# Performance work log

Measured on AMD Instinct MI355X. Metric: run time of the kernel, lower is better.

## Reference

```python
import jax, jax.numpy as jnp
import numpy as np

R = 40            # guided-filter radius (81x81 window)
EPS = 1e-3
BETA = 2.996 / 300.0  # visibility_m = 300.0


def _box_sum(x, r=R):
    """Zero-padded sliding-window sum over an (B,C,H,W) tensor.
    Matches F.avg_pool2d(x, 2r+1, stride=1, padding=r) * (2r+1)^2
    (count_include_pad=True), computed in O(HW) via prefix sums."""
    B, C, H, W = x.shape

    def _along(y, axis, L):
        cs = jnp.cumsum(y, axis=axis)
        pad = [(0, 0)] * 4
        pad[axis] = (1, 0)
        cs = jnp.pad(cs, pad)  # cs[i] = sum of first i elements
        hi = jnp.clip(jnp.arange(L) + r + 1, 0, L)
        lo = jnp.clip(jnp.arange(L) - r, 0, L)
        return jnp.take(cs, hi, axis=axis) - jnp.take(cs, lo, axis=axis)

    x = _along(x, 2, H)
    x = _along(x, 3, W)
    return x


def _guided_filter(I, p, r=R, eps=EPS):
    N = (2 * r + 1) ** 2
    mean_I = _box_sum(I, r) / N
    mean_p = _box_sum(p, r) / N
    mean_Ip = _box_sum(I * p, r) / N
    cov_Ip = mean_Ip - mean_I * mean_p
    mean_II = _box_sum(I * I, r) / N
    var_I = mean_II - mean_I * mean_I
    a = cov_Ip / (var_I + eps)
    b = mean_p - a * mean_I
    mean_a = _box_sum(a, r) / N
    mean_b = _box_sum(b, r) / N
    return mean_a * I + mean_b


def setup_inputs() -> dict:
    key = jax.random.key(0)
    k1, k2 = jax.random.split(key)
    B, H, W = 8, 768, 1280
    img = jax.random.uniform(k1, (B, 3, H, W), dtype=jnp.float32)
    depth = jax.random.uniform(k2, (B, 1, H, W), dtype=jnp.float32) * 500.0
    return {"img": img, "depth": depth}


def reference(img, depth):
    B, _, H, W = img.shape
    t_raw = jnp.clip(jnp.exp(-BETA * depth), 0.0, 1.0)          # (B,1,H,W)
    gray = (0.299 * img[:, 0:1] + 0.587 * img[:, 1:2]
            + 0.114 * img[:, 2:3])                               # (B,1,H,W)
    t = _guided_filter(gray, t_raw)                               # (B,1,H,W)

    # atmospheric light A: mean color over the k farthest pixels, per image
    k = max(10, int(0.001 * H * W))
    k = min(k, H * W)
    depth_flat = depth.reshape(B, -1)                             # (B,HW)
    img_flat = img.reshape(B, 3, -1)                              # (B,3,HW)
    _, idx = jax.lax.top_k(depth_flat, k)                         # (B,k)
    A = jnp.take_along_axis(img_flat, idx[:, None, :], axis=2).mean(axis=2)
    A = A.reshape(B, 3, 1, 1)

    return img * t + A * (1.0 - t)
```

## Files before the change

### kernel.cpp

```cpp
#include <hip/hip_runtime.h>
#include <hip/hip_fp16.h>
#include <stdint.h>

typedef unsigned int u32;

#define Bn 8
#define Hn 768
#define Wn 1280
#define HWs (Hn*Wn)
#define Rr 40
#define NNinv (1.0f/6561.0f)
#define KTOP 983
#define BETA_C (2.996f/300.0f)
#define EQCAP 4096
#define TK_BPI 480
#define NCH 96
#define SEGV 16
#define NSEGV 48
#define HIMG 4
#define TK1_WAVES 16
#define TW 640
#define CW 680

#define OFF_F     0
#define OFF_AB1   (16*HWs)
#define OFF_AB2   (24*HWs)
#define OFF_CS4f  (32*HWs)
#define OFF_CS2f  (36*HWs)
#define OFF_TAILf (38*HWs)

#define OFFH_FOVF 0
#define OFFH_AB   (4*HWs)
#define CS_N      (HIMG*NCH*Wn)
#define OFFH_CS4  (12*HWs)
#define OFFH_CS2  (OFFH_CS4 + 4*CS_N)
#define OFFH_TAIL (OFFH_CS2 + 2*CS_N)

#define ZERO_U32  (Bn*4096 + Bn*65536 + Bn)
#define ZERO_U4   (ZERO_U32/4)

__device__ __forceinline__ float4 f4add(float4 a, float4 b){ return make_float4(a.x+b.x,a.y+b.y,a.z+b.z,a.w+b.w); }
__device__ __forceinline__ float4 f4sub(float4 a, float4 b){ return make_float4(a.x-b.x,a.y-b.y,a.z-b.z,a.w-b.w); }

__device__ __forceinline__ u32 h2_to_u32(__half2 h){ union { __half2 h; u32 u; } c; c.h = h; return c.u; }
__device__ __forceinline__ __half2 u32_to_h2(u32 u){ union { u32 u; __half2 h; } c; c.u = u; return c.h; }

__global__ __launch_bounds__(256) void fill0_kernel(uint4* __restrict__ p){
  int i = blockIdx.x*256 + threadIdx.x;
  if (i < ZERO_U4) p[i] = make_uint4(0,0,0,0);
}


__global__ __launch_bounds__(256) void gA_kernel(const float* __restrict__ img, const float* __restrict__ depth,
    uint2* __restrict__ F, float4* __restrict__ CS4){
  __shared__ float4 lds[769];
  __shared__ float4 wtot[4];
  int blk = blockIdx.x;
  int xt = blk & 1;
  int t2 = blk >> 1;
  int b = t2 / NCH, ch = t2 % NCH;
  int x0 = xt*TW;
  int cstart = xt ? (TW - Rr) : 0;
  int tid = threadIdx.x;
  int lane = tid & 63, wv = tid >> 6;
  float4 acc[3];
  #pragma unroll
  for (int j = 0; j < 3; ++j) acc[j] = make_float4(0,0,0,0);
  for (int r = 0; r < 8; ++r){
    int y = ch*8 + r;
    const float* ir = img + ((size_t)(b*3+0)*Hn + y)*Wn + cstart;
    const float* ig = img + ((size_t)(b*3+1)*Hn + y)*Wn + cstart;
    const float* ib = img + ((size_t)(b*3+2)*Hn + y)*Wn + cstart;
    const float* dp = depth + ((size_t)b*Hn + y)*Wn + cstart;
    __syncthreads();
    for (int i = tid; i < 768; i += 256){
      if (i < CW){
        float rr = ir[i], g = ig[i], bb = ib[i];
        float I = 0.299f*rr + 0.587f*g + 0.114f*bb;
        float p = expf(-BETA_C*dp[i]);
        p = fminf(fmaxf(p, 0.0f), 1.0f);
        lds[i] = make_float4(I, p, I*p, I*I);
      } else {
        lds[i] = make_float4(0,0,0,0);
      }
    }
    __syncthreads();
    int base = tid*3;
    float4 loc[3]; float4 tsum = make_float4(0,0,0,0);
    #pragma unroll
    for (int j = 0; j < 3; ++j){ loc[j] = lds[base+j]; tsum = f4add(tsum, loc[j]); }
    float4 v = tsum;
    for (int d = 1; d < 64; d <<= 1){
      float4 o; o.x = __shfl_up(v.x, d); o.y = __shfl_up(v.y, d); o.z = __shfl_up(v.z, d); o.w = __shfl_up(v.w, d);
      if (lane >= d) v = f4add(v, o);
    }
    if (lane == 63) wtot[wv] = v;
    __syncthreads();
    float4 ex = f4sub(v, tsum);
    for (int w = 0; w < wv; ++w) ex = f4add(ex, wtot[w]);
    float4 run = ex;
    #pragma unroll
    for (int j = 0; j < 3; ++j){ lds[base+j] = run; run = f4add(run, loc[j]); }
    __syncthreads();
    #pragma unroll
    for (int j = 0; j < 3; ++j){
      int lx = tid + j*256;
      if (lx < TW){
        int gx = x0 + lx;
        int hi = gx + Rr + 1; if (hi > Wn) hi = Wn;
        int lo = gx - Rr;     if (lo < 0)  lo = 0;
        float4 s = f4sub(lds[hi - cstart], lds[lo - cstart]);
        __half2 h01 = __float22half2_rn(make_float2(s.x, s.y));
        __half2 h23 = __float22half2_rn(make_float2(s.z, s.w));
        F[(size_t)b*HWs + (size_t)y*Wn + gx] = make_uint2(h2_to_u32(h01), h2_to_u32(h23));
        float2 f0 = __half22float2(h01), f1 = __half22float2(h23);
        acc[j] = f4add(acc[j], make_float4(f0.x, f0.y, f1.x, f1.y));
      }
    }
  }
  #pragma unroll
  for (int j = 0; j < 3; ++j){
    int lx = tid + j*256;
    if (lx < TW) CS4[((size_t)b*NCH + ch)*Wn + x0 + lx] = acc[j];
  }
}

__global__ __launch_bounds__(256) void vAf_kernel(const uint2* __restrict__ F, const float4* __restrict__ CS,
    u32* __restrict__ AB){
  int gt = blockIdx.x*256 + threadIdx.x;
  int x  = gt % Wn;
  int t2 = gt / Wn;
  int b = t2 % Bn, s = t2 / Bn;
  const uint2* Fb   = F + (size_t)b*HWs;
  const float4* CSb = CS + (size_t)b*NCH*Wn;
  int y0 = s*SEGV;
  int c0 = 2*s - 5; if (c0 < 0) c0 = 0;
  int c1 = 2*s + 5; if (c1 > NCH) c1 = NCH;
  float4 S = make_float4(0,0,0,0);
  for (int c = c0; c < c1; ++c) S = f4add(S, CSb[(size_t)c*Wn + x]);
  u32* ABb = AB + (size_t)b*HWs;
  #pragma unroll 2
  for (int y = y0; y < y0 + SEGV; ++y){
    int ya = y + Rr;
    if (ya < Hn){
      uint2 u = Fb[(size_t)ya*Wn + x];
      float2 f0 = __half22float2(u32_to_h2(u.x)), f1 = __half22float2(u32_to_h2(u.y));
      S.x += f0.x; S.y += f0.y; S.z += f1.x; S.w += f1.y;
    }
    float mI = S.x*NNinv, mp = S.y*NNinv, mIp = S.z*NNinv, mII = S.w*NNinv;
    float var = mII - mI*mI;
    float a  = (mIp - mI*mp) / (var + 1e-3f);
    float bb = mp - a*mI;
    ABb[(size_t)y*Wn + x] = h2_to_u32(__float22half2_rn(make_float2(a, bb)));
    int yb = y - Rr;
    if (yb >= 0){
      uint2 u = Fb[(size_t)yb*Wn + x];
      float2 f0 = __half22float2(u32_to_h2(u.x)), f1 = __half22float2(u32_to_h2(u.y));
      S.x -= f0.x; S.y -= f0.y; S.z -= f1.x; S.w -= f1.y;
    }
  }
}

__global__ __launch_bounds__(256) void gB_kernel(const u32* __restrict__ AB1, u32* __restrict__ AB2,
    float2* __restrict__ CS2){
  __shared__ float2 lds[769];
  __shared__ float2 wtot[4];
  int blk = blockIdx.x;
  int xt = blk & 1;
  int t2 = blk >> 1;
  int b = t2 / NCH, ch = t2 % NCH;
  int x0 = xt*TW;
  int cstart = xt ? (TW - Rr) : 0;
  int tid = threadIdx.x;
  int lane = tid & 63, wv = tid >> 6;
  float2 acc[3];
  #pragma unroll
  for (int j = 0; j < 3; ++j) acc[j] = make_float2(0,0);
  for (int r = 0; r < 8; ++r){
    int y = ch*8 + r;
    const u32* row = AB1 + (size_t)b*HWs + (size_t)y*Wn + cstart;
    __syncthreads();
    for (int i = tid; i < 768; i += 256){
      if (i < CW) lds[i] = __half22float2(u32_to_h2(row[i]));
      else        lds[i] = make_float2(0,0);
    }
    __syncthreads();
    int base = tid*3;
    float2 loc[3]; float2 tsum = make_float2(0,0);
    #pragma unroll
    for (int j = 0; j < 3; ++j){ loc[j] = lds[base+j]; tsum.x += loc[j].x; tsum.y += loc[j].y; }
    float2 v = tsum;
    for (int d = 1; d < 64; d <<= 1){
      float2 o; o.x = __shfl_up(v.x, d); o.y = __shfl_up(v.y, d);
      if (lane >= d){ v.x += o.x; v.y += o.y; }
    }
    if (lane == 63) wtot[wv] = v;
    __syncthreads();
    float2 ex = make_float2(v.x - tsum.x, v.y - tsum.y);
    for (int w = 0; w < wv; ++w){ ex.x += wtot[w].x; ex.y += wtot[w].y; }
    float2 run = ex;
    #pragma unroll
    for (int j = 0; j < 3; ++j){ lds[base+j] = run; run.x += loc[j].x; run.y += loc[j].y; }
    __syncthreads();
    #pragma unroll
    for (int j = 0; j < 3; ++j){
      int lx = tid + j*256;
      if (lx < TW){
        int gx = x0 + lx;
        int hi = gx + Rr + 1; if (hi > Wn) hi = Wn;
        int lo = gx - Rr;     if (lo < 0)  lo = 0;
        float2 s = make_float2(lds[hi - cstart].x - lds[lo - cstart].x,
                               lds[hi - cstart].y - lds[lo - cstart].y);
        __half2 h = __float22half2_rn(s);
        AB2[(size_t)b*HWs + (size_t)y*Wn + gx] = h2_to_u32(h);
        float2 fr = __half22float2(h);
        acc[j].x += fr.x; acc[j].y += fr.y;
      }
    }
  }
  #pragma unroll
  for (int j = 0; j < 3; ++j){
    int lx = tid + j*256;
    if (lx < TW) CS2[((size_t)b*NCH + ch)*Wn + x0 + lx] = acc[j];
  }
}

__global__ __launch_bounds__(256) void vBf_kernel(const u32* __restrict__ AB2, const float2* __restrict__ CS,
    const float* __restrict__ img, const float* __restrict__ Avec, float* __restrict__ out){
  int gt = blockIdx.x*256 + threadIdx.x;
  int x  = gt % Wn;
  int t2 = gt / Wn;
  int b = t2 % Bn, s = t2 / Bn;
  const u32* ABb = AB2 + (size_t)b*HWs;
  const float2* CSb = CS + (size_t)b*NCH*Wn;
  int y0 = s*SEGV;
  int c0 = 2*s - 5; if (c0 < 0) c0 = 0;
  int c1 = 2*s + 5; if (c1 > NCH) c1 = NCH;
  float2 S = make_float2(0,0);
  for (int c = c0; c < c1; ++c){ float2 t = CSb[(size_t)c*Wn + x]; S.x += t.x; S.y += t.y; }
  float A0 = Avec[b*3+0], A1 = Avec[b*3+1], A2 = Avec[b*3+2];
  const float* ir = img + (size_t)(b*3+0)*HWs;
  const float* ig = img + (size_t)(b*3+1)*HWs;
  const float* ib = img + (size_t)(b*3+2)*HWs;
  float* o0 = out + (size_t)(b*3+0)*HWs;
  float* o1 = out + (size_t)(b*3+1)*HWs;
  float* o2 = out + (size_t)(b*3+2)*HWs;
  #pragma unroll 2
  for (int y = y0; y < y0 + SEGV; ++y){
    int ya = y + Rr;
    if (ya < Hn){ float2 t = __half22float2(u32_to_h2(ABb[(size_t)ya*Wn + x])); S.x += t.x; S.y += t.y; }
    float ma = S.x*NNinv, mb = S.y*NNinv;
    size_t idx = (size_t)y*Wn + x;
    float r = ir[idx], g = ig[idx], bb = ib[idx];
    float gray = 0.299f*r + 0.587f*g + 0.114f*bb;
    float t = ma*gray + mb;
    o0[idx] = r *t + A0*(1.0f - t);
    o1[idx] = g *t + A1*(1.0f - t);
    o2[idx] = bb*t + A2*(1.0f - t);
    int yb = y - Rr;
    if (yb >= 0){ float2 t2v = __half22float2(u32_to_h2(ABb[(size_t)yb*Wn + x])); S.x -= t2v.x; S.y -= t2v.y; }
  }
}


__global__ __launch_bounds__(256) void hA_kernel(const float* __restrict__ img, const float* __restrict__ depth,
    float4* __restrict__ Fd, float4* __restrict__ Fw, int half){
  __shared__ float4 lds[Wn+1];
  __shared__ float4 wtot[4];
  int blk = blockIdx.x;
  int bl = blk / Hn, y = blk % Hn;
  int b = half*HIMG + bl;
  const float* ir = img + ((size_t)(b*3+0)*Hn + y)*Wn;
  const float* ig = img + ((size_t)(b*3+1)*Hn + y)*Wn;
  const float* ib = img + ((size_t)(b*3+2)*Hn + y)*Wn;
  const float* dp = depth + ((size_t)b*Hn + y)*Wn;
  int tid = threadIdx.x;
  for (int i = tid; i < Wn; i += 256){
    float r = ir[i], g = ig[i], bb = ib[i];
    float I = 0.299f*r + 0.587f*g + 0.114f*bb;
    float p = expf(-BETA_C*dp[i]);
    p = fminf(fmaxf(p, 0.0f), 1.0f);
    lds[i] = make_float4(I, p, I*p, I*I);
  }
  __syncthreads();
  float4 loc[5]; float4 tsum = make_float4(0,0,0,0);
  for (int j = 0; j < 5; ++j){ loc[j] = lds[tid*5+j]; tsum = f4add(tsum, loc[j]); }
  int lane = tid & 63, wv = tid >> 6;
  float4 v = tsum;
  for (int d = 1; d < 64; d <<= 1){
    float4 o; o.x = __shfl_up(v.x, d); o.y = __shfl_up(v.y, d); o.z = __shfl_up(v.z, d); o.w = __shfl_up(v.w, d);
    if (lane >= d) v = f4add(v, o);
  }
  if (lane == 63) wtot[wv] = v;
  __syncthreads();
  float4 ex = f4sub(v, tsum);
  for (int w = 0; w < wv; ++w) ex = f4add(ex, wtot[w]);
  float4 run = ex;
  for (int j = 0; j < 5; ++j){ lds[tid*5+j] = run; run = f4add(run, loc[j]); }
  if (tid == 255) lds[Wn] = run;
  __syncthreads();
  float4* F = (bl < 3) ? (Fd + (size_t)bl*HWs) : Fw;
  for (int j = 0; j < 5; ++j){
    int xx = tid + j*256;
    int hi = xx + Rr + 1; if (hi > Wn) hi = Wn;
    int lo = xx - Rr;     if (lo < 0)  lo = 0;
    F[(size_t)y*Wn + xx] = f4sub(lds[hi], lds[lo]);
  }
}

__global__ __launch_bounds__(256) void cs4_kernel(const float4* __restrict__ Fd, const float4* __restrict__ Fw,
    float4* __restrict__ CS){
  int gt = blockIdx.x*256 + threadIdx.x;
  int x  = gt % Wn;
  int t2 = gt / Wn;
  int bl = t2 % HIMG, ch = t2 / HIMG;
  const float4* F = (bl < 3) ? (Fd + (size_t)bl*HWs) : Fw;
  const float4* p = F + (size_t)ch*8*Wn + x;
  float4 s = make_float4(0,0,0,0);
  #pragma unroll
  for (int i = 0; i < 8; ++i) s = f4add(s, p[(size_t)i*Wn]);
  CS[((size_t)bl*NCH + ch)*Wn + x] = s;
}

__global__ __launch_bounds__(256) void vA_kernel(const float4* __restrict__ Fd, const float4* __restrict__ Fw,
    const float4* __restrict__ CS, float2* __restrict__ AB){
  int gt = blockIdx.x*256 + threadIdx.x;
  int x  = gt % Wn;
  int t2 = gt / Wn;
  int bl = t2 % HIMG, s = t2 / HIMG;
  const float4* F   = (bl < 3) ? (Fd + (size_t)bl*HWs) : Fw;
  const float4* CSb = CS + (size_t)bl*NCH*Wn;
  int y0 = s*SEGV;
  int c0 = 2*s - 5; if (c0 < 0) c0 = 0;
  int c1 = 2*s + 5; if (c1 > NCH) c1 = NCH;
  float4 S = make_float4(0,0,0,0);
  for (int c = c0; c < c1; ++c) S = f4add(S, CSb[(size_t)c*Wn + x]);
  float2* ABb = AB + (size_t)bl*HWs;
  #pragma unroll 2
  for (int y = y0; y < y0 + SEGV; ++y){
    int ya = y + Rr;
    if (ya < Hn) S = f4add(S, F[(size_t)ya*Wn + x]);
    float mI = S.x*NNinv, mp = S.y*NNinv, mIp = S.z*NNinv, mII = S.w*NNinv;
    float var = mII - mI*mI;
    float a  = (mIp - mI*mp) / (var + 1e-3f);
    float bb = mp - a*mI;
    ABb[(size_t)y*Wn + x] = make_float2(a, bb);
    int yb = y - Rr;
    if (yb >= 0) S = f4sub(S, F[(size_t)yb*Wn + x]);
  }
}

__global__ __launch_bounds__(256) void hB_kernel(float2* __restrict__ AB){
  __shared__ float2 lds[Wn+1];
  __shared__ float2 wtot[4];
  int blk = blockIdx.x;
  int bl = blk / Hn, y = blk % Hn;
  float2* row = AB + ((size_t)bl*Hn + y)*Wn;
  int tid = threadIdx.x;
  for (int i = tid; i < Wn; i += 256) lds[i] = row[i];
  __syncthreads();
  float2 loc[5]; float2 tsum = make_float2(0,0);
  for (int j = 0; j < 5; ++j){ loc[j] = lds[tid*5+j]; tsum.x += loc[j].x; tsum.y += loc[j].y; }
  int lane = tid & 63, wv = tid >> 6;
  float2 v = tsum;
  for (int d = 1; d < 64; d <<= 1){
    float2 o; o.x = __shfl_up(v.x, d); o.y = __shfl_up(v.y, d);
    if (lane >= d){ v.x += o.x; v.y += o.y; }
  }
  if (lane == 63) wtot[wv] = v;
  __syncthreads();
  float2 ex = make_float2(v.x - tsum.x, v.y - tsum.y);
  for (int w = 0; w < wv; ++w){ ex.x += wtot[w].x; ex.y += wtot[w].y; }
  float2 run = ex;
  for (int j = 0; j < 5; ++j){ lds[tid*5+j] = run; run.x += loc[j].x; run.y += loc[j].y; }
  if (tid == 255) lds[Wn] = run;
  __syncthreads();
  for (int j = 0; j < 5; ++j){
    int xx = tid + j*256;
    int hi = xx + Rr + 1; if (hi > Wn) hi = Wn;
    int lo = xx - Rr;     if (lo < 0)  lo = 0;
    row[xx] = make_float2(lds[hi].x - lds[lo].x, lds[hi].y - lds[lo].y);
  }
}

__global__ __launch_bounds__(256) void cs2_kernel(const float2* __restrict__ AB, float2* __restrict__ CS){
  int gt = blockIdx.x*256 + threadIdx.x;
  int x  = gt % Wn;
  int t2 = gt / Wn;
  int bl = t2 % HIMG, ch = t2 / HIMG;
  const float2* p = AB + (size_t)bl*HWs + (size_t)ch*8*Wn + x;
  float2 s = make_float2(0,0);
  #pragma unroll
  for (int i = 0; i < 8; ++i){ s.x += p[(size_t)i*Wn].x; s.y += p[(size_t)i*Wn].y; }
  CS[((size_t)bl*NCH + ch)*Wn + x] = s;
}

__global__ __launch_bounds__(256) void vB_kernel(const float2* __restrict__ AB, const float2* __restrict__ CS,
    const float* __restrict__ img, const float* __restrict__ Avec, float* __restrict__ out, int half){
  int gt = blockIdx.x*256 + threadIdx.x;
  int x  = gt % Wn;
  int t2 = gt / Wn;
  int bl = t2 % HIMG, s = t2 / HIMG;
  int b = half*HIMG + bl;
  const float2* ABb = AB + (size_t)bl*HWs;
  const float2* CSb = CS + (size_t)bl*NCH*Wn;
  int y0 = s*SEGV;
  int c0 = 2*s - 5; if (c0 < 0) c0 = 0;
  int c1 = 2*s + 5; if (c1 > NCH) c1 = NCH;
  float2 S = make_float2(0,0);
  for (int c = c0; c < c1; ++c){ float2 t = CSb[(size_t)c*Wn + x]; S.x += t.x; S.y += t.y; }
  float A0 = Avec[b*3+0], A1 = Avec[b*3+1], A2 = Avec[b*3+2];
  const float* ir = img + (size_t)(b*3+0)*HWs;
  const float* ig = img + (size_t)(b*3+1)*HWs;
  const float* ib = img + (size_t)(b*3+2)*HWs;
  float* o0 = out + (size_t)(b*3+0)*HWs;
  float* o1 = out + (size_t)(b*3+1)*HWs;
  float* o2 = out + (size_t)(b*3+2)*HWs;
  #pragma unroll 2
  for (int y = y0; y < y0 + SEGV; ++y){
    int ya = y + Rr;
    if (ya < Hn){ float2 t = ABb[(size_t)ya*Wn + x]; S.x += t.x; S.y += t.y; }
    float ma = S.x*NNinv, mb = S.y*NNinv;
    size_t idx = (size_t)y*Wn + x;
    float r = ir[idx], g = ig[idx], bb = ib[idx];
    float gray = 0.299f*r + 0.587f*g + 0.114f*bb;
    float t = ma*gray + mb;
    o0[idx] = r *t + A0*(1.0f - t);
    o1[idx] = g *t + A1*(1.0f - t);
    o2[idx] = bb*t + A2*(1.0f - t);
    int yb = y - Rr;
    if (yb >= 0){ float2 t2v = ABb[(size_t)yb*Wn + x]; S.x -= t2v.x; S.y -= t2v.y; }
  }
}


__global__ __launch_bounds__(1024) void tk1_kernel(const float* __restrict__ depth, u32* __restrict__ hist1){
  __shared__ u32 lh[TK1_WAVES*2048];
  int tid = threadIdx.x;
  for (int i = tid; i < TK1_WAVES*2048; i += 1024) lh[i] = 0;
  __syncthreads();
  int b = blockIdx.x >> 5;
  int slice = blockIdx.x & 31;
  const int per = HWs/32;
  int start = b*HWs + slice*per;
  u32* h = &lh[(tid >> 6) * 2048];
  const float2* dp = (const float2*)(depth + start);
  for (int i = tid; i < per/2; i += 1024){
    float2 v = dp[i];
    u32 u0 = __float_as_uint(v.x), u1 = __float_as_uint(v.y);
    u32 b0 = u0 >> 20, b1 = u1 >> 20;
    atomicAdd(&h[b0 >> 1], (b0 & 1u) ? 65536u : 1u);
    atomicAdd(&h[b1 >> 1], (b1 & 1u) ? 65536u : 1u);
  }
  __syncthreads();
  for (int i = tid; i < 4096; i += 1024){
    u32 s = 0;
    for (int w = 0; w < TK1_WAVES; ++w) s += (lh[w*2048 + (i>>1)] >> ((i&1)*16)) & 0xFFFFu;
    if (s) atomicAdd(&hist1[b*4096+i], s);
  }
}

__global__ __launch_bounds__(256) void tk2_kernel(const u32* __restrict__ hist1,
    u32* __restrict__ selP1, u32* __restrict__ selK1){
  int b = blockIdx.x, tid = threadIdx.x;
  const u32* h = hist1 + b*4096;
  u32 cs = 0; int bb = tid*16;
  for (int i = 0; i < 16; ++i) cs += h[bb+i];
  __shared__ u32 sums[256];
  sums[tid] = cs; __syncthreads();
  u32 above = 0;
  for (int t = tid+1; t < 256; ++t) above += sums[t];
  if (above < KTOP && above + cs >= KTOP){
    u32 acc = above;
    for (int i = 15; i >= 0; --i){
      u32 c = h[bb+i]; acc += c;
      if (acc >= KTOP){ selP1[b] = (u32)(bb+i); selK1[b] = KTOP - (acc - c); break; }
    }
  }
}

__global__ __launch_bounds__(256) void tk3_kernel(const float* __restrict__ depth,
    const u32* __restrict__ selP1, u32* __restrict__ hist2){
  int idx = blockIdx.x*2048 + threadIdx.x;
  int b = blockIdx.x / TK_BPI;
  u32 p1 = selP1[b];
  for (int it = 0; it < 8; ++it, idx += 256){
    u32 u = __float_as_uint(depth[idx]);
    if ((u>>20) == p1) atomicAdd(&hist2[b*65536 + ((u>>4)&0xFFFFu)], 1u);
  }
}

__global__ __launch_bounds__(256) void tk4_kernel(const u32* __restrict__ hist2, const u32* __restrict__ selP1,
    const u32* __restrict__ selK1, u32* __restrict__ selTau, u32* __restrict__ selK2){
  int b = blockIdx.x, tid = threadIdx.x;
  const u32* h = hist2 + b*65536;
  u32 kk = selK1[b];
  u32 cs = 0; int bb = tid*256;
  for (int i = 0; i < 256; ++i) cs += h[bb+i];
  __shared__ u32 sums[256];
  sums[tid] = cs; __syncthreads();
  u32 above = 0;
  for (int t = tid+1; t < 256; ++t) above += sums[t];
  if (above < kk && above + cs >= kk){
    u32 acc = above;
    for (int i = 255; i >= 0; --i){
      u32 c = h[bb+i]; acc += c;
      if (acc >= kk){ selTau[b] = (selP1[b]<<16) | (u32)(bb+i); selK2[b] = kk - (acc - c); break; }
    }
  }
}

__global__ __launch_bounds__(256) void tk5_kernel(const float* __restrict__ depth, const float* __restrict__ img,
    const u32* __restrict__ selTau, u32* __restrict__ eqCount, u32* __restrict__ eqVal, u32* __restrict__ eqIdx,
    float* __restrict__ partial){
  int blk = blockIdx.x;
  int b = blk / TK_BPI;
  u32 tau = selTau[b];
  int idx = blk*2048 + threadIdx.x;
  float cr = 0.f, cg = 0.f, cb = 0.f;
  for (int it = 0; it < 8; ++it, idx += 256){
    int pix = idx - b*HWs;
    u32 u = __float_as_uint(depth[idx]);
    u32 u28 = u >> 4;
    if (u28 > tau){
      cr += img[(size_t)(b*3+0)*HWs + pix];
      cg += img[(size_t)(b*3+1)*HWs + pix];
      cb += img[(size_t)(b*3+2)*HWs + pix];
    } else if (u28 == tau){
      u32 p = atomicAdd(&eqCount[b], 1u);
      if (p < EQCAP){ eqVal[b*EQCAP+p] = u; eqIdx[b*EQCAP+p] = (u32)pix; }
    }
  }
  for (int d = 32; d; d >>= 1){
    cr += __shfl_down(cr, d); cg += __shfl_down(cg, d); cb += __shfl_down(cb, d);
  }
  __shared__ float wsum[4][3];
  int lane = threadIdx.x & 63, wv = threadIdx.x >> 6;
  if (lane == 0){ wsum[wv][0] = cr; wsum[wv][1] = cg; wsum[wv][2] = cb; }
  __syncthreads();
  if (threadIdx.x == 0){
    float r = 0.f, g = 0.f, bl = 0.f;
    for (int w = 0; w < 4; ++w){ r += wsum[w][0]; g += wsum[w][1]; bl += wsum[w][2]; }
    partial[blk*3+0] = r; partial[blk*3+1] = g; partial[blk*3+2] = bl;
  }
}

__global__ void tk6_kernel(const float* __restrict__ img, const u32* __restrict__ eqCount,
    u32* __restrict__ eqVal, const u32* __restrict__ eqIdx, const u32* __restrict__ selK2,
    const float* __restrict__ partial, float* __restrict__ Avec){
  int b = blockIdx.x;
  int tid = threadIdx.x;
  float r = 0.f, g = 0.f, bl = 0.f;
  for (int i = tid; i < TK_BPI; i += 64){
    r  += partial[(b*TK_BPI+i)*3+0];
    g  += partial[(b*TK_BPI+i)*3+1];
    bl += partial[(b*TK_BPI+i)*3+2];
  }
  for (int d = 32; d; d >>= 1){
    r += __shfl_down(r, d); g += __shfl_down(g, d); bl += __shfl_down(bl, d);
  }
  if (tid != 0) return;
  u32 m = eqCount[b]; if (m > EQCAP) m = EQCAP;
  u32 need = selK2[b]; if (need > m) need = m;
  float cr = r, cg = g, cb = bl;
  for (u32 it = 0; it < need; ++it){
    int best = -1; u32 bv = 0, bi = 0;
    for (u32 j = 0; j < m; ++j){
      u32 vv = eqVal[b*EQCAP+j];
      if (vv == 0xFFFFFFFFu) continue;
      u32 ix = eqIdx[b*EQCAP+j];
      if (best < 0 || vv > bv || (vv == bv && ix < bi)){ best = (int)j; bv = vv; bi = ix; }
    }
    eqVal[b*EQCAP+best] = 0xFFFFFFFFu;
    cr += img[(size_t)(b*3+0)*HWs + bi];
    cg += img[(size_t)(b*3+1)*HWs + bi];
    cb += img[(size_t)(b*3+2)*HWs + bi];
  }
  float inv = 1.0f/(float)KTOP;
  Avec[b*3+0] = cr*inv; Avec[b*3+1] = cg*inv; Avec[b*3+2] = cb*inv;
}


extern "C" void kernel_launch(void* const* d_in, const int* in_sizes, int n_in,
                              void* d_out, int out_size, void* d_ws, size_t ws_size,
                              hipStream_t stream){
  const float* img   = (const float*)d_in[0];
  const float* depth = (const float*)d_in[1];
  float* out = (float*)d_out;
  float* ws  = (float*)d_ws;

  const size_t tailFloats = (size_t)ZERO_U32 + 4*Bn + 2*(size_t)Bn*EQCAP
                          + (size_t)Bn*TK_BPI*3 + Bn*3 + 16;
  const size_t needFull = ((size_t)38*HWs + tailFloats) * sizeof(float);
  bool full = (ws_size >= needFull);

  size_t offTail = full ? (size_t)OFF_TAILf : (size_t)OFFH_TAIL;
  u32* tail    = (u32*)(ws + offTail);
  u32* hist1   = tail;
  u32* hist2   = hist1 + Bn*4096;
  u32* eqCount = hist2 + (size_t)Bn*65536;
  u32* selP1   = eqCount + Bn;
  u32* selK1   = selP1 + Bn;
  u32* selTau  = selK1 + Bn;
  u32* selK2   = selTau + Bn;
  u32* eqVal   = selK2 + Bn;
  u32* eqIdx   = eqVal + (size_t)Bn*EQCAP;
  float* partial = (float*)(eqIdx + (size_t)Bn*EQCAP);
  float* Avec    = partial + (size_t)Bn*TK_BPI*3;

  fill0_kernel<<<dim3((ZERO_U4 + 255)/256), dim3(256), 0, stream>>>((uint4*)tail);

  tk1_kernel<<<dim3(Bn*32), dim3(1024), 0, stream>>>(depth, hist1);
  tk2_kernel<<<dim3(Bn),    dim3(256), 0, stream>>>(hist1, selP1, selK1);
  tk3_kernel<<<dim3(Bn*TK_BPI), dim3(256), 0, stream>>>(depth, selP1, hist2);
  tk4_kernel<<<dim3(Bn),    dim3(256), 0, stream>>>(hist2, selP1, selK1, selTau, selK2);
  tk5_kernel<<<dim3(Bn*TK_BPI), dim3(256), 0, stream>>>(depth, img, selTau, eqCount, eqVal, eqIdx, partial);
  tk6_kernel<<<dim3(Bn),    dim3(64),  0, stream>>>(img, eqCount, eqVal, eqIdx, selK2, partial, Avec);

  if (full){
    uint2*  F   = (uint2*)(ws + OFF_F);
    u32*    AB1 = (u32*)(ws + OFF_AB1);
    u32*    AB2 = (u32*)(ws + OFF_AB2);
    float4* CS4 = (float4*)(ws + OFF_CS4f);
    float2* CS2 = (float2*)(ws + OFF_CS2f);
    gA_kernel <<<dim3(Bn*NCH*2),            dim3(256), 0, stream>>>(img, depth, F, CS4);
    vAf_kernel<<<dim3((Bn*Wn*NSEGV)/256),   dim3(256), 0, stream>>>(F, CS4, AB1);
    gB_kernel <<<dim3(Bn*NCH*2),            dim3(256), 0, stream>>>(AB1, AB2, CS2);
    vBf_kernel<<<dim3((Bn*Wn*NSEGV)/256),   dim3(256), 0, stream>>>(AB2, CS2, img, Avec, out);
  } else {
    float4* Fw  = (float4*)(ws + OFFH_FOVF);
    float2* AB  = (float2*)(ws + OFFH_AB);
    float4* CS4 = (float4*)(ws + OFFH_CS4);
    float2* CS2 = (float2*)(ws + OFFH_CS2);
    for (int half = 0; half < 2; ++half){
      float4* Fd = (float4*)out + (size_t)half*3*HWs;
      hA_kernel <<<dim3(HIMG*Hn),            dim3(256), 0, stream>>>(img, depth, Fd, Fw, half);
      cs4_kernel<<<dim3((HIMG*NCH*Wn)/256),  dim3(256), 0, stream>>>(Fd, Fw, CS4);
      vA_kernel <<<dim3((HIMG*Wn*NSEGV)/256),dim3(256), 0, stream>>>(Fd, Fw, CS4, AB);
      hB_kernel <<<dim3(HIMG*Hn),            dim3(256), 0, stream>>>(AB);
      cs2_kernel<<<dim3((HIMG*NCH*Wn)/256),  dim3(256), 0, stream>>>(AB, CS2);
      vB_kernel <<<dim3((HIMG*Wn*NSEGV)/256),dim3(256), 0, stream>>>(AB, CS2, img, Avec, out, half);
    }
  }
}
```

Measured before the change: 234.9 us.

## Compact top-k candidates in pass 3 and vectorize guided-filter input loads

The third top-k pass now also accumulates colour sums for pixels whose coarse bin is above the threshold. It compacts the pixels that fall in the threshold bin into a per-image candidate list through an LDS stage and one global atomic per block. The fifth pass then scans only that short candidate list with far fewer blocks, instead of re-reading the whole depth map. This removes a full depth pass and most of the image gathers, at the cost of more workspace for candidate buffers and extra atomics in tk3. Separately, gA loads image and depth as float2, with two pixels per thread, and zeroes the LDS tail in one step.

Result: slower. 250.0 us (+6.4%).

```diff
diff --git a/kernel.cpp b/kernel.cpp
--- a/kernel.cpp
+++ b/kernel.cpp
@@ -14,6 +14,9 @@
 #define BETA_C (2.996f/300.0f)
 #define EQCAP 4096
 #define TK_BPI 480
+#define TK5_BPI 64
+#define TK_PART (TK_BPI + TK5_BPI)
+#define CAND_CAP HWs
 #define NCH 96
 #define SEGV 16
 #define NSEGV 48
@@ -36,7 +39,7 @@
 #define OFFH_CS2  (OFFH_CS4 + 4*CS_N)
 #define OFFH_TAIL (OFFH_CS2 + 2*CS_N)
 
-#define ZERO_U32  (Bn*4096 + Bn*65536 + Bn)
+#define ZERO_U32  (Bn*4096 + Bn*65536 + Bn + Bn*32)
 #define ZERO_U4   (ZERO_U32/4)
 
 __device__ __forceinline__ float4 f4add(float4 a, float4 b){ return make_float4(a.x+b.x,a.y+b.y,a.z+b.z,a.w+b.w); }
@@ -68,22 +71,21 @@
   for (int j = 0; j < 3; ++j) acc[j] = make_float4(0,0,0,0);
   for (int r = 0; r < 8; ++r){
     int y = ch*8 + r;
-    const float* ir = img + ((size_t)(b*3+0)*Hn + y)*Wn + cstart;
-    const float* ig = img + ((size_t)(b*3+1)*Hn + y)*Wn + cstart;
-    const float* ib = img + ((size_t)(b*3+2)*Hn + y)*Wn + cstart;
-    const float* dp = depth + ((size_t)b*Hn + y)*Wn + cstart;
-    __syncthreads();
-    for (int i = tid; i < 768; i += 256){
-      if (i < CW){
-        float rr = ir[i], g = ig[i], bb = ib[i];
-        float I = 0.299f*rr + 0.587f*g + 0.114f*bb;
-        float p = expf(-BETA_C*dp[i]);
-        p = fminf(fmaxf(p, 0.0f), 1.0f);
-        lds[i] = make_float4(I, p, I*p, I*I);
-      } else {
-        lds[i] = make_float4(0,0,0,0);
-      }
-    }
+    const float2* ir2 = (const float2*)(img + ((size_t)(b*3+0)*Hn + y)*Wn + cstart);
+    const float2* ig2 = (const float2*)(img + ((size_t)(b*3+1)*Hn + y)*Wn + cstart);
+    const float2* ib2 = (const float2*)(img + ((size_t)(b*3+2)*Hn + y)*Wn + cstart);
+    const float2* dp2 = (const float2*)(depth + ((size_t)b*Hn + y)*Wn + cstart);
+    __syncthreads();
+    for (int i = tid; i < 340; i += 256){
+      float2 r2 = ir2[i], g2 = ig2[i], b2 = ib2[i], d2 = dp2[i];
+      float I0 = 0.299f*r2.x + 0.587f*g2.x + 0.114f*b2.x;
+      float I1 = 0.299f*r2.y + 0.587f*g2.y + 0.114f*b2.y;
+      float e0 = fminf(fmaxf(expf(-BETA_C*d2.x), 0.0f), 1.0f);
+      float e1 = fminf(fmaxf(expf(-BETA_C*d2.y), 0.0f), 1.0f);
+      lds[2*i]   = make_float4(I0, e0, I0*e0, I0*I0);
+      lds[2*i+1] = make_float4(I1, e1, I1*e1, I1*I1);
+    }
+    if (tid < 88) lds[680+tid] = make_float4(0,0,0,0);
     __syncthreads();
     int base = tid*3;
     float4 loc[3]; float4 tsum = make_float4(0,0,0,0);
@@ -479,14 +481,54 @@
   }
 }
 
-__global__ __launch_bounds__(256) void tk3_kernel(const float* __restrict__ depth,
-    const u32* __restrict__ selP1, u32* __restrict__ hist2){
-  int idx = blockIdx.x*2048 + threadIdx.x;
-  int b = blockIdx.x / TK_BPI;
+__global__ __launch_bounds__(256) void tk3_kernel(const float* __restrict__ depth, const float* __restrict__ img,
+    const u32* __restrict__ selP1, u32* __restrict__ hist2,
+    u32* __restrict__ candU, u32* __restrict__ candP, u32* __restrict__ candCnt,
+    float* __restrict__ partial){
+  __shared__ u32 lu[2048], lp[2048];
+  __shared__ u32 lcnt, gbase;
+  int blk = blockIdx.x;
+  int b = blk / TK_BPI;
+  int tid = threadIdx.x;
+  if (tid == 0) lcnt = 0;
+  __syncthreads();
   u32 p1 = selP1[b];
+  int idx = blk*2048 + tid;
+  float cr = 0.f, cg = 0.f, cb = 0.f;
   for (int it = 0; it < 8; ++it, idx += 256){
+    int pix = idx - b*HWs;
     u32 u = __float_as_uint(depth[idx]);
-    if ((u>>20) == p1) atomicAdd(&hist2[b*65536 + ((u>>4)&0xFFFFu)], 1u);
+    u32 bin = u >> 20;
+    if (bin > p1){
+      cr += img[(size_t)(b*3+0)*HWs + pix];
+      cg += img[(size_t)(b*3+1)*HWs + pix];
+      cb += img[(size_t)(b*3+2)*HWs + pix];
+    } else if (bin == p1){
+      atomicAdd(&hist2[b*65536 + ((u>>4)&0xFFFFu)], 1u);
+      u32 pos = atomicAdd(&lcnt, 1u);
+      lu[pos] = u; lp[pos] = (u32)pix;
+    }
+  }
+  __syncthreads();
+  if (tid == 0) gbase = atomicAdd(&candCnt[b*32], lcnt);
+  __syncthreads();
+  u32 n = lcnt, base = gbase;
+  for (u32 i = tid; i < n; i += 256){
+    candU[(size_t)b*CAND_CAP + base + i] = lu[i];
+    candP[(size_t)b*CAND_CAP + base + i] = lp[i];
+  }
+  for (int d = 32; d; d >>= 1){
+    cr += __shfl_down(cr, d); cg += __shfl_down(cg, d); cb += __shfl_down(cb, d);
+  }
+  __shared__ float wsum[4][3];
+  int lane = tid & 63, wv = tid >> 6;
+  if (lane == 0){ wsum[wv][0] = cr; wsum[wv][1] = cg; wsum[wv][2] = cb; }
+  __syncthreads();
+  if (tid == 0){
+    float r = 0.f, g = 0.f, bl = 0.f;
+    for (int w = 0; w < 4; ++w){ r += wsum[w][0]; g += wsum[w][1]; bl += wsum[w][2]; }
+    int slot = b*TK_PART + (blk - b*TK_BPI);
+    partial[slot*3+0] = r; partial[slot*3+1] = g; partial[slot*3+2] = bl;
   }
 }
 
@@ -510,17 +552,18 @@
   }
 }
 
-__global__ __launch_bounds__(256) void tk5_kernel(const float* __restrict__ depth, const float* __restrict__ img,
+__global__ __launch_bounds__(256) void tk5_kernel(const float* __restrict__ img,
+    const u32* __restrict__ candU, const u32* __restrict__ candP, const u32* __restrict__ candCnt,
     const u32* __restrict__ selTau, u32* __restrict__ eqCount, u32* __restrict__ eqVal, u32* __restrict__ eqIdx,
     float* __restrict__ partial){
-  int blk = blockIdx.x;
-  int b = blk / TK_BPI;
+  int b = blockIdx.x / TK5_BPI;
+  int lb = blockIdx.x % TK5_BPI;
   u32 tau = selTau[b];
-  int idx = blk*2048 + threadIdx.x;
+  u32 cnt = candCnt[b*32]; if (cnt > CAND_CAP) cnt = CAND_CAP;
   float cr = 0.f, cg = 0.f, cb = 0.f;
-  for (int it = 0; it < 8; ++it, idx += 256){
-    int pix = idx - b*HWs;
-    u32 u = __float_as_uint(depth[idx]);
+  for (u32 i = lb*256 + threadIdx.x; i < cnt; i += TK5_BPI*256){
+    u32 u = candU[(size_t)b*CAND_CAP + i];
+    u32 pix = candP[(size_t)b*CAND_CAP + i];
     u32 u28 = u >> 4;
     if (u28 > tau){
       cr += img[(size_t)(b*3+0)*HWs + pix];
@@ -528,7 +571,7 @@
       cb += img[(size_t)(b*3+2)*HWs + pix];
     } else if (u28 == tau){
       u32 p = atomicAdd(&eqCount[b], 1u);
-      if (p < EQCAP){ eqVal[b*EQCAP+p] = u; eqIdx[b*EQCAP+p] = (u32)pix; }
+      if (p < EQCAP){ eqVal[b*EQCAP+p] = u; eqIdx[b*EQCAP+p] = pix; }
     }
   }
   for (int d = 32; d; d >>= 1){
@@ -541,7 +584,8 @@
   if (threadIdx.x == 0){
     float r = 0.f, g = 0.f, bl = 0.f;
     for (int w = 0; w < 4; ++w){ r += wsum[w][0]; g += wsum[w][1]; bl += wsum[w][2]; }
-    partial[blk*3+0] = r; partial[blk*3+1] = g; partial[blk*3+2] = bl;
+    int slot = b*TK_PART + TK_BPI + lb;
+    partial[slot*3+0] = r; partial[slot*3+1] = g; partial[slot*3+2] = bl;
   }
 }
 
@@ -551,10 +595,10 @@
   int b = blockIdx.x;
   int tid = threadIdx.x;
   float r = 0.f, g = 0.f, bl = 0.f;
-  for (int i = tid; i < TK_BPI; i += 64){
-    r  += partial[(b*TK_BPI+i)*3+0];
-    g  += partial[(b*TK_BPI+i)*3+1];
-    bl += partial[(b*TK_BPI+i)*3+2];
+  for (int i = tid; i < TK_PART; i += 64){
+    r  += partial[(b*TK_PART+i)*3+0];
+    g  += partial[(b*TK_PART+i)*3+1];
+    bl += partial[(b*TK_PART+i)*3+2];
   }
   for (int d = 32; d; d >>= 1){
     r += __shfl_down(r, d); g += __shfl_down(g, d); bl += __shfl_down(bl, d);
@@ -590,7 +634,8 @@
   float* ws  = (float*)d_ws;
 
   const size_t tailFloats = (size_t)ZERO_U32 + 4*Bn + 2*(size_t)Bn*EQCAP
-                          + (size_t)Bn*TK_BPI*3 + Bn*3 + 16;
+                          + (size_t)Bn*TK_PART*3 + Bn*3
+                          + 2*(size_t)Bn*CAND_CAP + 16;
   const size_t needFull = ((size_t)38*HWs + tailFloats) * sizeof(float);
   bool full = (ws_size >= needFull);
 
@@ -599,22 +644,25 @@
   u32* hist1   = tail;
   u32* hist2   = hist1 + Bn*4096;
   u32* eqCount = hist2 + (size_t)Bn*65536;
-  u32* selP1   = eqCount + Bn;
+  u32* candCnt = eqCount + Bn;
+  u32* selP1   = candCnt + Bn*32;
   u32* selK1   = selP1 + Bn;
   u32* selTau  = selK1 + Bn;
   u32* selK2   = selTau + Bn;
   u32* eqVal   = selK2 + Bn;
   u32* eqIdx   = eqVal + (size_t)Bn*EQCAP;
   float* partial = (float*)(eqIdx + (size_t)Bn*EQCAP);
-  float* Avec    = partial + (size_t)Bn*TK_BPI*3;
+  float* Avec    = partial + (size_t)Bn*TK_PART*3;
+  u32* candU   = (u32*)(Avec + Bn*3);
+  u32* candP   = candU + (size_t)Bn*CAND_CAP;
 
   fill0_kernel<<<dim3((ZERO_U4 + 255)/256), dim3(256), 0, stream>>>((uint4*)tail);
 
   tk1_kernel<<<dim3(Bn*32), dim3(1024), 0, stream>>>(depth, hist1);
   tk2_kernel<<<dim3(Bn),    dim3(256), 0, stream>>>(hist1, selP1, selK1);
-  tk3_kernel<<<dim3(Bn*TK_BPI), dim3(256), 0, stream>>>(depth, selP1, hist2);
+  tk3_kernel<<<dim3(Bn*TK_BPI), dim3(256), 0, stream>>>(depth, img, selP1, hist2, candU, candP, candCnt, partial);
   tk4_kernel<<<dim3(Bn),    dim3(256), 0, stream>>>(hist2, selP1, selK1, selTau, selK2);
-  tk5_kernel<<<dim3(Bn*TK_BPI), dim3(256), 0, stream>>>(depth, img, selTau, eqCount, eqVal, eqIdx, partial);
+  tk5_kernel<<<dim3(Bn*TK5_BPI), dim3(256), 0, stream>>>(img, candU, candP, candCnt, selTau, eqCount, eqVal, eqIdx, partial);
   tk6_kernel<<<dim3(Bn),    dim3(64),  0, stream>>>(img, eqCount, eqVal, eqIdx, selK2, partial, Avec);
 
   if (full){
```
